# Kernel optimization log

Hardware: AMD Instinct MI355X
Metric: run time of the kernel (lower is better)

Reference implementation:

```python
import jax, jax.numpy as jnp
import numpy as np

NUM_TAGS = 64
PAD, BOS, EOS = 0, 1, 2
B, S = 256, 2048


def setup_inputs() -> dict:
    key = jax.random.key(0)
    k1, k2, k3 = jax.random.split(key, 3)
    C = NUM_TAGS
    emissions = jax.random.normal(k1, (B, S, C), dtype=jnp.float32)
    # left-contiguous mask (1=keep), lengths in [S//2, S]
    lengths = jax.random.randint(k2, (B,), S // 2, S + 1)
    mask = (jnp.arange(S)[None, :] < lengths[:, None]).astype(jnp.float32)
    # transitions initialized as in CRF.__init__
    t = np.asarray(jax.random.normal(k3, (C, C), dtype=jnp.float32)).copy()
    t[:, BOS] = -10000.0
    t[EOS, :] = -10000.0
    t[:, PAD] = -10000.0
    t[PAD, :] = -10000.0
    t[PAD, PAD] = 0.0
    t[PAD, EOS] = 0.0
    transitions = jnp.asarray(t, dtype=jnp.float32)
    return {"emissions": emissions, "mask": mask, "transitions": transitions}


def reference(emissions, mask, transitions):
    # Viterbi decode. Returns best tag path per sample, padded with PAD to
    # length S (original pads to max path length, which is data-dependent;
    # under jit we pad to S -- valid entries are identical).
    Bn, Sn, C = emissions.shape
    lengths = mask.sum(axis=1).astype(jnp.int32)  # [B]

    alpha0 = emissions[:, 0] + transitions[BOS][None, :]  # [B,C]

    def fwd_step(alpha, x):
        emit, m = x  # emit: [B,C], m: [B]
        scores = alpha[:, :, None] + transitions[None]  # [B, prev C, cur C]
        best = scores.max(axis=1)                       # [B,C]
        bt = scores.argmax(axis=1).astype(jnp.int32)    # [B,C] backpointers
        new_alpha = best + emit
        alpha = jnp.where(m[:, None] > 0, new_alpha, alpha)
        return alpha, bt

    xs = (emissions[:, 1:].swapaxes(0, 1), mask[:, 1:].swapaxes(0, 1))
    alpha, bps = jax.lax.scan(fwd_step, alpha0, xs)  # bps: [S-1, B, C]

    alpha = alpha + transitions[:, EOS][None, :]
    best_last = alpha.argmax(axis=1).astype(jnp.int32)  # [B]

    # vectorized backtrace: t runs S-2 .. 0; only active while t <= len-2
    def back_step(cur, x):
        t, bp = x  # bp: [B,C]
        new = jnp.take_along_axis(bp, cur[:, None], axis=1)[:, 0]
        active = t <= (lengths - 2)
        cur = jnp.where(active, new, cur)
        return cur, cur

    ts = jnp.arange(Sn - 1)
    _, ys = jax.lax.scan(back_step, best_last, (ts, bps), reverse=True)
    body = ys.swapaxes(0, 1)  # [B, S-1], body[:, t] = tag at position t

    full = jnp.concatenate([body, jnp.zeros((Bn, 1), body.dtype)], axis=1)  # [B,S]
    pos = jnp.arange(Sn)[None, :]
    out = jnp.where(pos < (lengths - 1)[:, None], full, PAD)
    out = out.at[jnp.arange(Bn), lengths - 1].set(best_last)
    return out.astype(jnp.int64)
```

## Files before the change

### kernel.cpp

```cpp
#include <hip/hip_runtime.h>

#define NBATCH 256
#define SLEN   2048
#define NTAG   64
#define BOS_T  1
#define EOS_T  2

#define BT_BYTES  131072
#define RING_ROWS 16
#define RING_BYTES (RING_ROWS * NTAG * 4)
#define FLAG_OFF  (BT_BYTES + RING_BYTES)
#define PROG_OFF  (FLAG_OFF + 16)
#define LDS_BYTES (PROG_OFF + 16)

typedef float f32x4 __attribute__((ext_vector_type(4)));

#define TAGS_ALL(X) \
  X(0)  X(1)  X(2)  X(3)  X(4)  X(5)  X(6)  X(7)  \
  X(8)  X(9)  X(10) X(11) X(12) X(13) X(14) X(15) \
  X(16) X(17) X(18) X(19) X(20) X(21) X(22) X(23) \
  X(24) X(25) X(26) X(27) X(28) X(29) X(30) X(31) \
  X(32) X(33) X(34) X(35) X(36) X(37) X(38) X(39) \
  X(40) X(41) X(42) X(43) X(44) X(45) X(46) X(47) \
  X(48) X(49) X(50) X(51) X(52) X(53) X(54) X(55) \
  X(56) X(57) X(58) X(59) X(60) X(61) X(62) X(63)

#define DECL_TC(p) float tc##p = trans[(p) * NTAG + lane];
#define KEEP_TC(p) asm volatile("" : "+v"(tc##p));

#define Q_ALL(X) X(0) X(1) X(2) X(3) X(4) X(5) X(6) X(7) \
                 X(8) X(9) X(10) X(11) X(12) X(13) X(14) X(15)
#define DECL_RR(q) f32x4 rr##q = rp[q];

#define MKCD(q, a0, a1, a2, a3) \
  float cd##a0 = rr##q[0] + tc##a0; float cd##a1 = rr##q[1] + tc##a1; \
  float cd##a2 = rr##q[2] + tc##a2; float cd##a3 = rr##q[3] + tc##a3;
#define ALL_CD() \
  MKCD(0,0,1,2,3)      MKCD(1,4,5,6,7)      MKCD(2,8,9,10,11)    MKCD(3,12,13,14,15) \
  MKCD(4,16,17,18,19)  MKCD(5,20,21,22,23)  MKCD(6,24,25,26,27)  MKCD(7,28,29,30,31) \
  MKCD(8,32,33,34,35)  MKCD(9,36,37,38,39)  MKCD(10,40,41,42,43) MKCD(11,44,45,46,47) \
  MKCD(12,48,49,50,51) MKCD(13,52,53,54,55) MKCD(14,56,57,58,59) MKCD(15,60,61,62,63)

#define FM3(x, y, z) fmaxf(fmaxf((x), (y)), (z))

#define LEAF(i, pa, pb) \
  float va##i; int ia##i; { bool g_ = (cd##pa >= cd##pb); \
    va##i = g_ ? cd##pa : cd##pb; ia##i = g_ ? (pa) : (pb); }
#define MRG(vo, io, vA, iA, vB, iB) \
  float vo; int io; { bool g_ = ((vA) >= (vB)); \
    vo = g_ ? (vA) : (vB); io = g_ ? (iA) : (iB); }

__global__ __launch_bounds__(256)
__attribute__((amdgpu_waves_per_eu(1, 1)))
void crf_viterbi(const float* __restrict__ emissions,
                 const float* __restrict__ mask,
                 const float* __restrict__ trans,
                 int* __restrict__ out)
{
    extern __shared__ unsigned char lds[];
    unsigned char* bt = lds;
    float* ring = (float*)(lds + BT_BYTES);
    volatile unsigned* flg = (volatile unsigned*)(lds + FLAG_OFF);
    volatile unsigned* prg = (volatile unsigned*)(lds + PROG_OFF);

    const int b    = blockIdx.x;
    const int tid  = threadIdx.x;
    const int w    = tid >> 6;
    const int lane = tid & 63;

    if (tid == 0) flg[0] = 0u;
    if (tid >= 1 && tid <= 3) prg[tid] = 0u;
    __syncthreads();

    TAGS_ALL(DECL_TC)

    const float* mrow = mask + (size_t)b * SLEN;
    float msum = 0.f;
    #pragma unroll
    for (int k = 0; k < SLEN / 64; ++k) msum += mrow[lane + k * 64];
    #pragma unroll
    for (int off = 32; off >= 1; off >>= 1) msum += __shfl_xor(msum, off, 64);
    const int len = (int)msum;

    const float* E = emissions + (size_t)b * SLEN * NTAG;
    int* orow = out + (size_t)b * SLEN;

    if (w == 0) {
        float a = E[lane] + tc1;
        ring[lane] = a;
        asm volatile("" ::: "memory");
        if (lane == 0) flg[0] = 1u;

        float e0 = E[NTAG + lane];
        float e1 = E[((2 < len) ? 2 : (len - 1)) * NTAG + lane];
        float e2 = E[((3 < len) ? 3 : (len - 1)) * NTAG + lane];
        float e3 = E[((4 < len) ? 4 : (len - 1)) * NTAG + lane];

        for (int t = 1; t < len; ++t) {
            TAGS_ALL(KEEP_TC)

            float emit = e0; e0 = e1; e1 = e2; e2 = e3;
            int tn = (t + 4 < len) ? (t + 4) : (len - 1);
            e3 = E[tn * NTAG + lane];

            const f32x4* rp = (const f32x4*)(ring + ((t - 1) & (RING_ROWS - 1)) * NTAG);
            Q_ALL(DECL_RR)
            ALL_CD()

            float l0  = FM3(cd0,  cd1,  cd2);
            float l1  = FM3(cd3,  cd4,  cd5);
            float l2  = FM3(cd6,  cd7,  cd8);
            float l3  = FM3(cd9,  cd10, cd11);
            float l4  = FM3(cd12, cd13, cd14);
            float l5  = FM3(cd15, cd16, cd17);
            float l6  = FM3(cd18, cd19, cd20);
            float l7  = FM3(cd21, cd22, cd23);
            float l8  = FM3(cd24, cd25, cd26);
            float l9  = FM3(cd27, cd28, cd29);
            float l10 = FM3(cd30, cd31, cd32);
            float l11 = FM3(cd33, cd34, cd35);
            float l12 = FM3(cd36, cd37, cd38);
            float l13 = FM3(cd39, cd40, cd41);
            float l14 = FM3(cd42, cd43, cd44);
            float l15 = FM3(cd45, cd46, cd47);
            float l16 = FM3(cd48, cd49, cd50);
            float l17 = FM3(cd51, cd52, cd53);
            float l18 = FM3(cd54, cd55, cd56);
            float l19 = FM3(cd57, cd58, cd59);
            float l20 = FM3(cd60, cd61, cd62);
            float m0 = FM3(l0,  l1,  l2);
            float m1 = FM3(l3,  l4,  l5);
            float m2 = FM3(l6,  l7,  l8);
            float m3 = FM3(l9,  l10, l11);
            float m4 = FM3(l12, l13, l14);
            float m5 = FM3(l15, l16, l17);
            float m6 = FM3(l18, l19, l20);
            float n0 = FM3(m0, m1, m2);
            float n1 = FM3(m3, m4, m5);
            float mx = fmaxf(FM3(n0, n1, m6), cd63);

            a = mx + emit;
            ring[(t & (RING_ROWS - 1)) * NTAG + lane] = a;
            asm volatile("" ::: "memory");
            if (lane == 0) flg[0] = (unsigned)(t + 1);

            if ((t & 7) == 0) {
                int g = 0;
                for (;;) {
                    unsigned m1_ = prg[1], m2_ = prg[2], m3_ = prg[3];
                    unsigned mn = m1_ < m2_ ? m1_ : m2_;
                    mn = mn < m3_ ? mn : m3_;
                    if ((int)mn >= t - 8 || ++g > 2000000) break;
                    __builtin_amdgcn_s_sleep(2);
                }
            }
        }

        float fin = a + trans[lane * NTAG + EOS_T];
        float v = fin; int idx = lane;
        #pragma unroll
        for (int off = 1; off < 64; off <<= 1) {
            float ov = __shfl_xor(v, off, 64);
            int   oi = __shfl_xor(idx, off, 64);
            if (ov > v || (ov == v && oi < idx)) { v = ov; idx = oi; }
        }
        int cur = idx;

        for (int i = len + lane; i < SLEN; i += 64) orow[i] = 0;
        if (lane == 0) orow[len - 1] = cur;

        {
            int g = 0;
            for (;;) {
                unsigned m1_ = prg[1], m2_ = prg[2], m3_ = prg[3];
                unsigned mn = m1_ < m2_ ? m1_ : m2_;
                mn = mn < m3_ ? mn : m3_;
                if (mn == 0x7fffffffu || ++g > 2000000) break;
                __builtin_amdgcn_s_sleep(2);
            }
        }
        asm volatile("" ::: "memory");

        for (int t = len - 2; t >= 0; --t) {
            cur = bt[t * NTAG + cur];
            if (lane == 0) orow[t] = cur;
        }
    } else {
        for (int t = w; t < len; t += 3) {
            TAGS_ALL(KEEP_TC)
            int g = 0;
            while (flg[0] < (unsigned)t) {
                __builtin_amdgcn_s_sleep(2);
                if (++g > 2000000) break;
            }
            asm volatile("" ::: "memory");

            const f32x4* rp = (const f32x4*)(ring + ((t - 1) & (RING_ROWS - 1)) * NTAG);
            Q_ALL(DECL_RR)
            ALL_CD()

            LEAF(0,  0,  1)  LEAF(1,  2,  3)  LEAF(2,  4,  5)  LEAF(3,  6,  7)
            LEAF(4,  8,  9)  LEAF(5,  10, 11) LEAF(6,  12, 13) LEAF(7,  14, 15)
            LEAF(8,  16, 17) LEAF(9,  18, 19) LEAF(10, 20, 21) LEAF(11, 22, 23)
            LEAF(12, 24, 25) LEAF(13, 26, 27) LEAF(14, 28, 29) LEAF(15, 30, 31)
            LEAF(16, 32, 33) LEAF(17, 34, 35) LEAF(18, 36, 37) LEAF(19, 38, 39)
            LEAF(20, 40, 41) LEAF(21, 42, 43) LEAF(22, 44, 45) LEAF(23, 46, 47)
            LEAF(24, 48, 49) LEAF(25, 50, 51) LEAF(26, 52, 53) LEAF(27, 54, 55)
            LEAF(28, 56, 57) LEAF(29, 58, 59) LEAF(30, 60, 61) LEAF(31, 62, 63)
            MRG(vb0,  ib0,  va0,  ia0,  va1,  ia1)   MRG(vb1,  ib1,  va2,  ia2,  va3,  ia3)
            MRG(vb2,  ib2,  va4,  ia4,  va5,  ia5)   MRG(vb3,  ib3,  va6,  ia6,  va7,  ia7)
            MRG(vb4,  ib4,  va8,  ia8,  va9,  ia9)   MRG(vb5,  ib5,  va10, ia10, va11, ia11)
            MRG(vb6,  ib6,  va12, ia12, va13, ia13)  MRG(vb7,  ib7,  va14, ia14, va15, ia15)
            MRG(vb8,  ib8,  va16, ia16, va17, ia17)  MRG(vb9,  ib9,  va18, ia18, va19, ia19)
            MRG(vb10, ib10, va20, ia20, va21, ia21)  MRG(vb11, ib11, va22, ia22, va23, ia23)
            MRG(vb12, ib12, va24, ia24, va25, ia25)  MRG(vb13, ib13, va26, ia26, va27, ia27)
            MRG(vb14, ib14, va28, ia28, va29, ia29)  MRG(vb15, ib15, va30, ia30, va31, ia31)
            MRG(vc0, ic0, vb0,  ib0,  vb1,  ib1)     MRG(vc1, ic1, vb2,  ib2,  vb3,  ib3)
            MRG(vc2, ic2, vb4,  ib4,  vb5,  ib5)     MRG(vc3, ic3, vb6,  ib6,  vb7,  ib7)
            MRG(vc4, ic4, vb8,  ib8,  vb9,  ib9)     MRG(vc5, ic5, vb10, ib10, vb11, ib11)
            MRG(vc6, ic6, vb12, ib12, vb13, ib13)    MRG(vc7, ic7, vb14, ib14, vb15, ib15)
            MRG(vd0, id0, vc0, ic0, vc1, ic1)        MRG(vd1, id1, vc2, ic2, vc3, ic3)
            MRG(vd2, id2, vc4, ic4, vc5, ic5)        MRG(vd3, id3, vc6, ic6, vc7, ic7)
            MRG(ve0, ie0, vd0, id0, vd1, id1)        MRG(ve1, ie1, vd2, id2, vd3, id3)
            MRG(vf0, if0, ve0, ie0, ve1, ie1)

            bt[(t - 1) * NTAG + lane] = (unsigned char)if0;
            asm volatile("" ::: "memory");
            prg[w] = (unsigned)t;
        }
        asm volatile("s_waitcnt lgkmcnt(0)" ::: "memory");
        prg[w] = 0x7fffffffu;
    }
}

extern "C" void kernel_launch(void* const* d_in, const int* in_sizes, int n_in,
                              void* d_out, int out_size, void* d_ws, size_t ws_size,
                              hipStream_t stream) {
    const float* emissions = (const float*)d_in[0];
    const float* mask      = (const float*)d_in[1];
    const float* trans     = (const float*)d_in[2];
    int* out = (int*)d_out;

    (void)hipFuncSetAttribute((const void*)crf_viterbi,
                              hipFuncAttributeMaxDynamicSharedMemorySize,
                              LDS_BYTES);

    crf_viterbi<<<NBATCH, 256, LDS_BYTES, stream>>>(emissions, mask, trans, out);
}
```

Before: 905.6 us.

## Parallelize Viterbi backtrace via chunked map composition across all waves

Replaces the serial single-wave backtrace with a three-phase parallel scheme. First, all waves compute per-chunk tag maps over 32-step chunks for every start tag. Then one wave composes the chunk maps to get each chunk's boundary tag, and finally all waves re-walk the chunks in parallel to write the outputs. It also packs the transition registers as float2 pairs for packed adds in the forward max, doubles the ring buffer to loosen producer/consumer coupling, and lengthens the sleep intervals. The cost is extra LDS, three block barriers, and roughly twice the backtrace LDS reads.

```diff
diff --git a/kernel.cpp b/kernel.cpp
--- a/kernel.cpp
+++ b/kernel.cpp
@@ -7,41 +7,42 @@
 #define EOS_T  2
 
 #define BT_BYTES  131072
-#define RING_ROWS 16
+#define RING_ROWS 32
 #define RING_BYTES (RING_ROWS * NTAG * 4)
 #define FLAG_OFF  (BT_BYTES + RING_BYTES)
-#define PROG_OFF  (FLAG_OFF + 16)
-#define LDS_BYTES (PROG_OFF + 16)
-
+#define PRG_OFF   (FLAG_OFF + 16)
+#define MAPS_OFF  (PRG_OFF + 16)
+#define BTAG_OFF  (MAPS_OFF + 4096)
+#define LDS_BYTES (BTAG_OFF + 272)
+
+typedef float f32x2 __attribute__((ext_vector_type(2)));
 typedef float f32x4 __attribute__((ext_vector_type(4)));
 
-#define TAGS_ALL(X) \
-  X(0)  X(1)  X(2)  X(3)  X(4)  X(5)  X(6)  X(7)  \
-  X(8)  X(9)  X(10) X(11) X(12) X(13) X(14) X(15) \
-  X(16) X(17) X(18) X(19) X(20) X(21) X(22) X(23) \
-  X(24) X(25) X(26) X(27) X(28) X(29) X(30) X(31) \
-  X(32) X(33) X(34) X(35) X(36) X(37) X(38) X(39) \
-  X(40) X(41) X(42) X(43) X(44) X(45) X(46) X(47) \
-  X(48) X(49) X(50) X(51) X(52) X(53) X(54) X(55) \
-  X(56) X(57) X(58) X(59) X(60) X(61) X(62) X(63)
-
-#define DECL_TC(p) float tc##p = trans[(p) * NTAG + lane];
-#define KEEP_TC(p) asm volatile("" : "+v"(tc##p));
-
-#define Q_ALL(X) X(0) X(1) X(2) X(3) X(4) X(5) X(6) X(7) \
-                 X(8) X(9) X(10) X(11) X(12) X(13) X(14) X(15)
+#define Q16(X) X(0) X(1) X(2) X(3) X(4) X(5) X(6) X(7) \
+               X(8) X(9) X(10) X(11) X(12) X(13) X(14) X(15)
+
+#define DECL_TP(q) \
+  f32x2 tpA##q = { trans[(4*(q)+0)*NTAG + lane], trans[(4*(q)+1)*NTAG + lane] }; \
+  f32x2 tpB##q = { trans[(4*(q)+2)*NTAG + lane], trans[(4*(q)+3)*NTAG + lane] };
+#define KEEP_TP(q) asm volatile("" : "+v"(tpA##q), "+v"(tpB##q));
+
 #define DECL_RR(q) f32x4 rr##q = rp[q];
 
+#define PKC(q) \
+  f32x2 cpA##q = (f32x2){rr##q[0], rr##q[1]} + tpA##q; \
+  f32x2 cpB##q = (f32x2){rr##q[2], rr##q[3]} + tpB##q; \
+  float qm##q = fmaxf(fmaxf(fmaxf(cpA##q[0], cpA##q[1]), cpB##q[0]), cpB##q[1]);
+
+#define FM3(x, y, z) fmaxf(fmaxf((x), (y)), (z))
+
 #define MKCD(q, a0, a1, a2, a3) \
-  float cd##a0 = rr##q[0] + tc##a0; float cd##a1 = rr##q[1] + tc##a1; \
-  float cd##a2 = rr##q[2] + tc##a2; float cd##a3 = rr##q[3] + tc##a3;
+  float cd##a0 = rr##q[0] + tpA##q[0]; float cd##a1 = rr##q[1] + tpA##q[1]; \
+  float cd##a2 = rr##q[2] + tpB##q[0]; float cd##a3 = rr##q[3] + tpB##q[1];
 #define ALL_CD() \
   MKCD(0,0,1,2,3)      MKCD(1,4,5,6,7)      MKCD(2,8,9,10,11)    MKCD(3,12,13,14,15) \
   MKCD(4,16,17,18,19)  MKCD(5,20,21,22,23)  MKCD(6,24,25,26,27)  MKCD(7,28,29,30,31) \
   MKCD(8,32,33,34,35)  MKCD(9,36,37,38,39)  MKCD(10,40,41,42,43) MKCD(11,44,45,46,47) \
   MKCD(12,48,49,50,51) MKCD(13,52,53,54,55) MKCD(14,56,57,58,59) MKCD(15,60,61,62,63)
-
-#define FM3(x, y, z) fmaxf(fmaxf((x), (y)), (z))
 
 #define LEAF(i, pa, pb) \
   float va##i; int ia##i; { bool g_ = (cd##pa >= cd##pb); \
@@ -58,10 +59,12 @@
                  int* __restrict__ out)
 {
     extern __shared__ unsigned char lds[];
-    unsigned char* bt = lds;
-    float* ring = (float*)(lds + BT_BYTES);
+    unsigned char* bt   = lds;
+    float*         ring = (float*)(lds + BT_BYTES);
     volatile unsigned* flg = (volatile unsigned*)(lds + FLAG_OFF);
-    volatile unsigned* prg = (volatile unsigned*)(lds + PROG_OFF);
+    volatile unsigned* prg = (volatile unsigned*)(lds + PRG_OFF);
+    unsigned char* maps = lds + MAPS_OFF;
+    int*           btag = (int*)(lds + BTAG_OFF);
 
     const int b    = blockIdx.x;
     const int tid  = threadIdx.x;
@@ -72,7 +75,7 @@
     if (tid >= 1 && tid <= 3) prg[tid] = 0u;
     __syncthreads();
 
-    TAGS_ALL(DECL_TC)
+    Q16(DECL_TP)
 
     const float* mrow = mask + (size_t)b * SLEN;
     float msum = 0.f;
@@ -81,12 +84,13 @@
     #pragma unroll
     for (int off = 32; off >= 1; off >>= 1) msum += __shfl_xor(msum, off, 64);
     const int len = (int)msum;
+    const int K   = (len - 1 + 31) >> 5;
 
     const float* E = emissions + (size_t)b * SLEN * NTAG;
     int* orow = out + (size_t)b * SLEN;
 
     if (w == 0) {
-        float a = E[lane] + tc1;
+        float a = E[lane] + tpA0[1];
         ring[lane] = a;
         asm volatile("" ::: "memory");
         if (lane == 0) flg[0] = 1u;
@@ -97,47 +101,22 @@
         float e3 = E[((4 < len) ? 4 : (len - 1)) * NTAG + lane];
 
         for (int t = 1; t < len; ++t) {
-            TAGS_ALL(KEEP_TC)
-
             float emit = e0; e0 = e1; e1 = e2; e2 = e3;
             int tn = (t + 4 < len) ? (t + 4) : (len - 1);
             e3 = E[tn * NTAG + lane];
 
             const f32x4* rp = (const f32x4*)(ring + ((t - 1) & (RING_ROWS - 1)) * NTAG);
-            Q_ALL(DECL_RR)
-            ALL_CD()
-
-            float l0  = FM3(cd0,  cd1,  cd2);
-            float l1  = FM3(cd3,  cd4,  cd5);
-            float l2  = FM3(cd6,  cd7,  cd8);
-            float l3  = FM3(cd9,  cd10, cd11);
-            float l4  = FM3(cd12, cd13, cd14);
-            float l5  = FM3(cd15, cd16, cd17);
-            float l6  = FM3(cd18, cd19, cd20);
-            float l7  = FM3(cd21, cd22, cd23);
-            float l8  = FM3(cd24, cd25, cd26);
-            float l9  = FM3(cd27, cd28, cd29);
-            float l10 = FM3(cd30, cd31, cd32);
-            float l11 = FM3(cd33, cd34, cd35);
-            float l12 = FM3(cd36, cd37, cd38);
-            float l13 = FM3(cd39, cd40, cd41);
-            float l14 = FM3(cd42, cd43, cd44);
-            float l15 = FM3(cd45, cd46, cd47);
-            float l16 = FM3(cd48, cd49, cd50);
-            float l17 = FM3(cd51, cd52, cd53);
-            float l18 = FM3(cd54, cd55, cd56);
-            float l19 = FM3(cd57, cd58, cd59);
-            float l20 = FM3(cd60, cd61, cd62);
-            float m0 = FM3(l0,  l1,  l2);
-            float m1 = FM3(l3,  l4,  l5);
-            float m2 = FM3(l6,  l7,  l8);
-            float m3 = FM3(l9,  l10, l11);
-            float m4 = FM3(l12, l13, l14);
-            float m5 = FM3(l15, l16, l17);
-            float m6 = FM3(l18, l19, l20);
-            float n0 = FM3(m0, m1, m2);
-            float n1 = FM3(m3, m4, m5);
-            float mx = fmaxf(FM3(n0, n1, m6), cd63);
+            Q16(DECL_RR)
+            Q16(PKC)
+
+            float s0 = FM3(qm0,  qm1,  qm2);
+            float s1 = FM3(qm3,  qm4,  qm5);
+            float s2 = FM3(qm6,  qm7,  qm8);
+            float s3 = FM3(qm9,  qm10, qm11);
+            float s4 = FM3(qm12, qm13, qm14);
+            float u0 = FM3(s0, s1, s2);
+            float u1 = fmaxf(s3, s4);
+            float mx = FM3(u0, u1, qm15);
 
             a = mx + emit;
             ring[(t & (RING_ROWS - 1)) * NTAG + lane] = a;
@@ -150,10 +129,11 @@
                     unsigned m1_ = prg[1], m2_ = prg[2], m3_ = prg[3];
                     unsigned mn = m1_ < m2_ ? m1_ : m2_;
                     mn = mn < m3_ ? mn : m3_;
-                    if ((int)mn >= t - 8 || ++g > 2000000) break;
-                    __builtin_amdgcn_s_sleep(2);
+                    if ((int)mn >= t - 16 || ++g > 2000000) break;
+                    __builtin_amdgcn_s_sleep(8);
                 }
             }
+            Q16(KEEP_TP)
         }
 
         float fin = a + trans[lane * NTAG + EOS_T];
@@ -164,39 +144,24 @@
             int   oi = __shfl_xor(idx, off, 64);
             if (ov > v || (ov == v && oi < idx)) { v = ov; idx = oi; }
         }
-        int cur = idx;
+        int best_last = idx;
 
         for (int i = len + lane; i < SLEN; i += 64) orow[i] = 0;
-        if (lane == 0) orow[len - 1] = cur;
-
-        {
-            int g = 0;
-            for (;;) {
-                unsigned m1_ = prg[1], m2_ = prg[2], m3_ = prg[3];
-                unsigned mn = m1_ < m2_ ? m1_ : m2_;
-                mn = mn < m3_ ? mn : m3_;
-                if (mn == 0x7fffffffu || ++g > 2000000) break;
-                __builtin_amdgcn_s_sleep(2);
-            }
-        }
-        asm volatile("" ::: "memory");
-
-        for (int t = len - 2; t >= 0; --t) {
-            cur = bt[t * NTAG + cur];
-            if (lane == 0) orow[t] = cur;
+        if (lane == 0) {
+            orow[len - 1] = best_last;
+            btag[K] = best_last;
         }
     } else {
         for (int t = w; t < len; t += 3) {
-            TAGS_ALL(KEEP_TC)
             int g = 0;
             while (flg[0] < (unsigned)t) {
-                __builtin_amdgcn_s_sleep(2);
-                if (++g > 2000000) break;
+                __builtin_amdgcn_s_sleep(16);
+                if (++g > 200000) break;
             }
             asm volatile("" ::: "memory");
 
             const f32x4* rp = (const f32x4*)(ring + ((t - 1) & (RING_ROWS - 1)) * NTAG);
-            Q_ALL(DECL_RR)
+            Q16(DECL_RR)
             ALL_CD()
 
             LEAF(0,  0,  1)  LEAF(1,  2,  3)  LEAF(2,  4,  5)  LEAF(3,  6,  7)
@@ -227,9 +192,54 @@
             bt[(t - 1) * NTAG + lane] = (unsigned char)if0;
             asm volatile("" ::: "memory");
             prg[w] = (unsigned)t;
-        }
-        asm volatile("s_waitcnt lgkmcnt(0)" ::: "memory");
-        prg[w] = 0x7fffffffu;
+            Q16(KEEP_TP)
+        }
+    }
+
+    __syncthreads();
+
+    {
+        #define C16(X) X(0) X(1) X(2) X(3) X(4) X(5) X(6) X(7) \
+                       X(8) X(9) X(10) X(11) X(12) X(13) X(14) X(15)
+        #define DECLCUR(i) \
+          const int k##i = w + 4*(i); const int base##i = k##i << 5; \
+          int top##i = base##i + 32; if (top##i > len - 1) top##i = len - 1; \
+          const int steps##i = (k##i < K) ? (top##i - base##i) : 0; \
+          int cur##i = lane;
+        C16(DECLCUR)
+        for (int j = 0; j < 32; ++j) {
+            #define STEPC(i) if (j < steps##i) \
+                cur##i = bt[(top##i - 1 - j) * NTAG + cur##i];
+            C16(STEPC)
+        }
+        #define STOREM(i) if (k##i < K) maps[(k##i << 6) + lane] = (unsigned char)cur##i;
+        C16(STOREM)
+    }
+    __syncthreads();
+
+    if (w == 0) {
+        int cur = btag[K];
+        for (int k = K - 1; k >= 0; --k) {
+            cur = maps[(k << 6) + cur];
+            if (lane == 0) btag[k] = cur;
+        }
+    }
+    __syncthreads();
+
+    {
+        #define DECLR(i) \
+          const int rk##i = w + 4*(i); const int rb##i = rk##i << 5; \
+          int rt##i = rb##i + 32; if (rt##i > len - 1) rt##i = len - 1; \
+          const int rs##i = (rk##i < K) ? (rt##i - rb##i) : 0; \
+          int rc##i = (rk##i < K) ? btag[rk##i + 1] : 0;
+        C16(DECLR)
+        for (int j = 0; j < 32; ++j) {
+            #define STEPR(i) if (j < rs##i) { \
+                const int t_ = rt##i - 1 - j; \
+                rc##i = bt[t_ * NTAG + rc##i]; \
+                if (lane == 0) orow[t_] = rc##i; }
+            C16(STEPR)
+        }
     }
 }
 
```

New measurement: 791.4 us. 1.14x faster.
